# Performance work log

Measured on AMD Instinct MI355X. Metric: run time of the kernel, lower is better.

## Reference

```python
import jax, jax.numpy as jnp
import numpy as np

N_NODES = 100000
N_EDGES = 1250000
IN_NDIM = 128
OUT_NDIM = 64


def setup_inputs() -> dict:
    key = jax.random.key(0)
    ks = jax.random.split(key, 8)
    return {
        "node_feats": jax.random.normal(ks[0], (N_NODES, IN_NDIM), dtype=jnp.float32),
        "edge_d": jax.random.uniform(ks[1], (N_EDGES, 1), dtype=jnp.float32),
        "W0": jax.random.normal(ks[2], (1, 1), dtype=jnp.float32),
        "W1": jax.random.normal(ks[3], (OUT_NDIM, IN_NDIM), dtype=jnp.float32) * (IN_NDIM ** -0.5),
        "W2": jax.random.normal(ks[4], (OUT_NDIM, IN_NDIM), dtype=jnp.float32) * (IN_NDIM ** -0.5),
        "Wa": jax.random.normal(ks[5], (1, 2 * OUT_NDIM + 1), dtype=jnp.float32) * (OUT_NDIM ** -0.5),
        "src": jax.random.randint(ks[6], (N_EDGES,), 0, N_NODES, dtype=jnp.int32),
        "dst": jax.random.randint(ks[7], (N_EDGES,), 0, N_NODES, dtype=jnp.int32),
    }


def reference(node_feats, edge_d, W0, W1, W2, Wa, src, dst):
    N = node_feats.shape[0]
    # fc1 / fc2 node projections (bias-free linears)
    z = node_feats @ W1.T            # [N, out_ndim]
    z_i = node_feats @ W2.T          # [N, out_ndim]
    # fc0 edge feature projection
    t = edge_d @ W0.T                # [E, 1]
    # gather per-edge endpoint features
    z_src = z[src]                   # [E, out_ndim]
    z_dst = z[dst]                   # [E, out_ndim]
    # attention logit: leaky_relu(attn_fc([z_src, z_dst, t]))
    a = jnp.concatenate([z_src, z_dst, t], axis=1) @ Wa.T   # [E, 1]
    e = jax.nn.leaky_relu(a[:, 0], 0.01)                      # torch default slope
    # segment softmax over incoming edges of each dst node
    m = jax.ops.segment_max(e, dst, num_segments=N)          # -inf for empty segs
    ex = jnp.exp(e - m[dst])
    denom = jax.ops.segment_sum(ex, dst, num_segments=N)
    alpha = ex / denom[dst]                                   # [E]
    # weighted scatter-sum of source messages
    z_neighbor = jax.ops.segment_sum(alpha[:, None] * z_src, dst, num_segments=N)
    h = jax.nn.relu(z_i + z_neighbor)
    return h
```

## Files before the change

### kernel.cpp

```cpp
#include <hip/hip_runtime.h>

#define N_NODES 100000
#define N_EDGES 1250000
#define IN_D 128
#define OUT_D 64
#define BSHIFT 8
#define NBUCK  391
#define CAP    4608
#define EPB    4096
#define NBLK_E 306
#define NBLK_G 1563

typedef __attribute__((ext_vector_type(8))) __bf16 bf16x8;
typedef __attribute__((ext_vector_type(4))) float floatx4;

__device__ __forceinline__ float2 up2(unsigned u) {
    return make_float2(__uint_as_float(u << 16),
                       __uint_as_float(u & 0xFFFF0000u));
}

__global__ __launch_bounds__(256) void fusedA_kernel(
    const float* __restrict__ x, const float* __restrict__ W1,
    const float* __restrict__ W2, const float* __restrict__ W0,
    const float* __restrict__ Wa,
    const int* __restrict__ dst, const int* __restrict__ src,
    const float* __restrict__ edge_d,
    int* __restrict__ gcur, uint2* __restrict__ payA,
    unsigned short* __restrict__ zb, unsigned short* __restrict__ zib,
    float* __restrict__ s1, float* __restrict__ s2)
{
    __shared__ __bf16 sB[16384];
    __shared__ float  sWa[128];
    __shared__ int    h[NBUCK];
    __shared__ int    lcur[NBUCK];

    const int t = threadIdx.x;

    if (blockIdx.x < NBLK_E) {
        const float tc = W0[0] * Wa[2 * OUT_D];
        for (int i = t; i < NBUCK; i += 256) h[i] = 0;
        __syncthreads();
        const int base = blockIdx.x * EPB;
        for (int k0 = 0; k0 < EPB; k0 += 1024) {
            int i = base + k0 + t * 4;
            if (i < N_EDGES) {
                int4 d4 = *(const int4*)(dst + i);
                atomicAdd(&h[d4.x >> BSHIFT], 1);
                atomicAdd(&h[d4.y >> BSHIFT], 1);
                atomicAdd(&h[d4.z >> BSHIFT], 1);
                atomicAdd(&h[d4.w >> BSHIFT], 1);
            }
        }
        __syncthreads();
        for (int b = t; b < NBUCK; b += 256) {
            int hc = h[b];
            int p = hc ? atomicAdd(&gcur[b], hc) : 0;
            lcur[b] = b * CAP + p;
        }
        __syncthreads();
        #define EMIT(dv, sv, ev)                                              \
            { int bk = (dv) >> BSHIFT;                                        \
              int pos = atomicAdd(&lcur[bk], 1);                              \
              if (pos < (bk + 1) * CAP)                                       \
                  payA[pos] = make_uint2((unsigned)(sv) |                     \
                                         ((unsigned)((dv) & 255) << 17),      \
                                         __float_as_uint(tc * (ev))); }
        for (int k0 = 0; k0 < EPB; k0 += 1024) {
            int i = base + k0 + t * 4;
            if (i < N_EDGES) {
                int4   d4 = *(const int4*)(dst + i);
                int4   s4 = *(const int4*)(src + i);
                float4 e4 = *(const float4*)(edge_d + i);
                EMIT(d4.x, s4.x, e4.x);
                EMIT(d4.y, s4.y, e4.y);
                EMIT(d4.z, s4.z, e4.z);
                EMIT(d4.w, s4.w, e4.w);
            }
        }
        #undef EMIT
        return;
    }

    #pragma unroll
    for (int g = 0; g < 8; ++g) {
        int gi = t + g * 256;
        int n  = gi >> 4;
        int k8 = gi & 15;
        const float* wrow = (n < 64) ? (W1 + n * 128) : (W2 + (n - 64) * 128);
        float4 v0 = *(const float4*)(wrow + k8 * 8);
        float4 v1 = *(const float4*)(wrow + k8 * 8 + 4);
        int lane = ((k8 & 3) << 4) | (n & 15);
        int off  = (((n >> 4) * 4 + (k8 >> 2)) * 64 + lane) * 8;
        bf16x8 bb;
        bb[0] = (__bf16)v0.x; bb[1] = (__bf16)v0.y;
        bb[2] = (__bf16)v0.z; bb[3] = (__bf16)v0.w;
        bb[4] = (__bf16)v1.x; bb[5] = (__bf16)v1.y;
        bb[6] = (__bf16)v1.z; bb[7] = (__bf16)v1.w;
        *(bf16x8*)(sB + off) = bb;
    }
    if (t < 128) sWa[t] = Wa[t];
    __syncthreads();

    const int lane = t & 63;
    const int wave = t >> 6;
    const int tile = (blockIdx.x - NBLK_E) * 4 + wave;
    if (tile * 16 >= N_NODES) return;

    const int n0 = tile * 16;
    const int m  = lane & 15;
    const int kb = lane >> 4;

    floatx4 acc[8];
    #pragma unroll
    for (int q = 0; q < 8; ++q) acc[q] = (floatx4)(0.f);

    const float* xrow = x + (size_t)(n0 + m) * IN_D;

    #pragma unroll
    for (int kc = 0; kc < 4; ++kc) {
        float4 v0 = *(const float4*)(xrow + kc * 32 + kb * 8);
        float4 v1 = *(const float4*)(xrow + kc * 32 + kb * 8 + 4);
        float xs[8] = {v0.x, v0.y, v0.z, v0.w, v1.x, v1.y, v1.z, v1.w};
        bf16x8 ahi, alo;
        #pragma unroll
        for (int j = 0; j < 8; ++j) {
            __bf16 hh = (__bf16)xs[j];
            ahi[j] = hh;
            alo[j] = (__bf16)(xs[j] - (float)hh);
        }
        #pragma unroll
        for (int nt = 0; nt < 8; ++nt) {
            int off = ((nt * 4 + kc) * 64 + lane) * 8;
            bf16x8 b = *(const bf16x8*)(sB + off);
            acc[nt] = __builtin_amdgcn_mfma_f32_16x16x32_bf16(ahi, b, acc[nt], 0, 0, 0);
            acc[nt] = __builtin_amdgcn_mfma_f32_16x16x32_bf16(alo, b, acc[nt], 0, 0, 0);
        }
    }

    #pragma unroll
    for (int nt = 0; nt < 8; ++nt) {
        int col = (nt & 3) * 16 + m;
        unsigned short* dp = (nt < 4) ? zb : zib;
        #pragma unroll
        for (int reg = 0; reg < 4; ++reg) {
            int row = n0 + kb * 4 + reg;
            __bf16 hh = (__bf16)acc[nt][reg];
            dp[(size_t)row * OUT_D + col] = *(unsigned short*)&hh;
        }
    }

    #pragma unroll
    for (int reg = 0; reg < 4; ++reg) {
        float p1 = 0.f, p2 = 0.f;
        #pragma unroll
        for (int nt = 0; nt < 4; ++nt) {
            float zv = acc[nt][reg];
            p1 += zv * sWa[nt * 16 + m];
            p2 += zv * sWa[64 + nt * 16 + m];
        }
        #pragma unroll
        for (int off = 8; off > 0; off >>= 1) {
            p1 += __shfl_xor(p1, off);
            p2 += __shfl_xor(p2, off);
        }
        if (m == 0) {
            int row = n0 + kb * 4 + reg;
            s1[row] = p1;
            s2[row] = p2;
        }
    }
}

__global__ __launch_bounds__(512) void passB_kernel(
    const int* __restrict__ gcur, const uint2* __restrict__ payA,
    int2* __restrict__ node_meta, uint2* __restrict__ payB)
{
    __shared__ int h[256];
    __shared__ int lc[256];
    __shared__ int sm[256];

    const int b = blockIdx.x, t = threadIdx.x;
    const int base = b * CAP;
    const int cnt = min(gcur[b], CAP);
    const int n0 = b << BSHIFT;

    if (t < 256) h[t] = 0;
    __syncthreads();

    for (int i0 = t * 4; i0 < cnt; i0 += 2048) {
        uint4 u0 = *(const uint4*)(payA + base + i0);
        uint4 u1 = *(const uint4*)(payA + base + i0 + 2);
        atomicAdd(&h[(u0.x >> 17) & 255], 1);
        if (i0 + 1 < cnt) atomicAdd(&h[(u0.z >> 17) & 255], 1);
        if (i0 + 2 < cnt) atomicAdd(&h[(u1.x >> 17) & 255], 1);
        if (i0 + 3 < cnt) atomicAdd(&h[(u1.z >> 17) & 255], 1);
    }
    __syncthreads();

    if (t < 256) {
        int v = h[t];
        sm[t] = v;
        __syncthreads();
        for (int off = 1; off < 256; off <<= 1) {
            int add = (t >= off) ? sm[t - off] : 0;
            __syncthreads();
            sm[t] += add;
            __syncthreads();
        }
        int start = base + sm[t] - v;
        lc[t] = start;
        if (n0 + t < N_NODES) node_meta[n0 + t] = make_int2(start, v);
    } else {
        __syncthreads();
        for (int off = 1; off < 256; off <<= 1) {
            __syncthreads(); __syncthreads();
        }
    }
    __syncthreads();

    #define PUT(xx, yy, ok)                                                   \
        if (ok) { int j = ((xx) >> 17) & 255;                                 \
                  int pos = atomicAdd(&lc[j], 1);                             \
                  payB[pos] = make_uint2((xx) & 0x1FFFFu, (yy)); }
    for (int i0 = t * 4; i0 < cnt; i0 += 2048) {
        uint4 u0 = *(const uint4*)(payA + base + i0);
        uint4 u1 = *(const uint4*)(payA + base + i0 + 2);
        PUT(u0.x, u0.y, true);
        PUT(u0.z, u0.w, i0 + 1 < cnt);
        PUT(u1.x, u1.y, i0 + 2 < cnt);
        PUT(u1.z, u1.w, i0 + 3 < cnt);
    }
    #undef PUT
}

__global__ __launch_bounds__(256) void gather_finalize_kernel(
    const int2* __restrict__ node_meta, const uint2* __restrict__ payB,
    const float* __restrict__ s1, const float* __restrict__ s2,
    const unsigned short* __restrict__ zb, const unsigned short* __restrict__ zib,
    float* __restrict__ out)
{
    __shared__ uint2 buf[8][32];

    const int lane = threadIdx.x & 63;
    const int wave = threadIdx.x >> 6;
    const int half = lane >> 5;
    const int lh   = lane & 31;
    const int nodeSlot = wave * 2 + half;
    const int d = blockIdx.x * 8 + nodeSlot;

    const int2 meta = node_meta[d];
    const int beg = meta.x;
    const int len = meta.y;
    const float s2d = s2[d];

    const int eC = lh >> 3;
    const int c  = lh & 7;

    float den = 0.f;
    float2 a0 = make_float2(0.f, 0.f), a1 = a0, a2 = a0, a3 = a0;

    for (int o = 0; o < len; o += 32) {
        int rem = len - o;
        bool v = lh < rem;
        uint2 p = payB[beg + o + (v ? lh : 0)];
        float ex = 0.f;
        if (v) {
            float a = __uint_as_float(p.y) + s1[p.x] + s2d;
            float e = (a > 0.f) ? a : 0.01f * a;
            ex = __expf(e);
            buf[nodeSlot][lh] = make_uint2(p.x, __float_as_uint(ex));
        }
        den += ex;

        int cnt = min(32, rem);
        for (int g = 0; g * 4 < cnt; ++g) {
            int j = g * 4 + eC;
            uint2 pe = buf[nodeSlot][(j < cnt) ? j : 0];
            float exe = (j < cnt) ? __uint_as_float(pe.y) : 0.f;
            uint4 zv = *(const uint4*)(zb + (size_t)pe.x * OUT_D + c * 8);
            float2 w0 = up2(zv.x), w1 = up2(zv.y), w2 = up2(zv.z), w3 = up2(zv.w);
            a0.x = fmaf(exe, w0.x, a0.x); a0.y = fmaf(exe, w0.y, a0.y);
            a1.x = fmaf(exe, w1.x, a1.x); a1.y = fmaf(exe, w1.y, a1.y);
            a2.x = fmaf(exe, w2.x, a2.x); a2.y = fmaf(exe, w2.y, a2.y);
            a3.x = fmaf(exe, w3.x, a3.x); a3.y = fmaf(exe, w3.y, a3.y);
        }
    }

    #pragma unroll
    for (int off = 16; off > 0; off >>= 1) den += __shfl_xor(den, off);
    #pragma unroll
    for (int off = 8; off <= 16; off <<= 1) {
        a0.x += __shfl_xor(a0.x, off); a0.y += __shfl_xor(a0.y, off);
        a1.x += __shfl_xor(a1.x, off); a1.y += __shfl_xor(a1.y, off);
        a2.x += __shfl_xor(a2.x, off); a2.y += __shfl_xor(a2.y, off);
        a3.x += __shfl_xor(a3.x, off); a3.y += __shfl_xor(a3.y, off);
    }

    if (lh < 8) {
        float inv = (den > 0.f) ? 1.f / den : 0.f;
        uint4 zv = *(const uint4*)(zib + (size_t)d * OUT_D + lh * 8);
        float2 w0 = up2(zv.x), w1 = up2(zv.y), w2 = up2(zv.z), w3 = up2(zv.w);
        float4 o0, o1;
        o0.x = fmaxf(w0.x + a0.x * inv, 0.f);
        o0.y = fmaxf(w0.y + a0.y * inv, 0.f);
        o0.z = fmaxf(w1.x + a1.x * inv, 0.f);
        o0.w = fmaxf(w1.y + a1.y * inv, 0.f);
        o1.x = fmaxf(w2.x + a2.x * inv, 0.f);
        o1.y = fmaxf(w2.y + a2.y * inv, 0.f);
        o1.z = fmaxf(w3.x + a3.x * inv, 0.f);
        o1.w = fmaxf(w3.y + a3.y * inv, 0.f);
        *(float4*)(out + (size_t)d * OUT_D + lh * 8)     = o0;
        *(float4*)(out + (size_t)d * OUT_D + lh * 8 + 4) = o1;
    }
}

extern "C" void kernel_launch(void* const* d_in, const int* in_sizes, int n_in,
                              void* d_out, int out_size, void* d_ws, size_t ws_size,
                              hipStream_t stream) {
    const float* node_feats = (const float*)d_in[0];
    const float* edge_d     = (const float*)d_in[1];
    const float* W0         = (const float*)d_in[2];
    const float* W1         = (const float*)d_in[3];
    const float* W2         = (const float*)d_in[4];
    const float* Wa         = (const float*)d_in[5];
    const int*   src        = (const int*)d_in[6];
    const int*   dst        = (const int*)d_in[7];
    float* out = (float*)d_out;

    char* ws = (char*)d_ws;
    uint2* payA = (uint2*)ws;    ws += (size_t)NBUCK * CAP * 8;
    uint2* payB = (uint2*)ws;    ws += (size_t)NBUCK * CAP * 8;
    unsigned short* zbuf = (unsigned short*)ws; ws += (size_t)N_NODES * OUT_D * 2;
    unsigned short* zib  = (unsigned short*)ws; ws += (size_t)N_NODES * OUT_D * 2;
    float* s1 = (float*)ws;      ws += (size_t)N_NODES * 4;
    float* s2 = (float*)ws;      ws += (size_t)N_NODES * 4;
    int2*  node_meta = (int2*)ws; ws += (size_t)N_NODES * 8;
    int*   gcur = (int*)ws;      ws += ((NBUCK + 3) & ~3) * 4;

    hipMemsetAsync(gcur, 0, NBUCK * 4, stream);

    fusedA_kernel<<<NBLK_E + NBLK_G, 256, 0, stream>>>(
        node_feats, W1, W2, W0, Wa, dst, src, edge_d,
        gcur, payA, zbuf, zib, s1, s2);

    passB_kernel<<<NBUCK, 512, 0, stream>>>(gcur, payA, node_meta, payB);

    gather_finalize_kernel<<<N_NODES / 8, 256, 0, stream>>>(
        node_meta, payB, s1, s2, zbuf, zib, out);
}
```

Before: 191.2 us.

## Fuse bucket sort and gather into one kernel with LDS-resident edge buckets

The second-pass counting sort is merged with the per-node softmax/gather kernel, so each 128-node bucket is sorted into shared memory and consumed in place rather than written to payB and node_meta in global memory. Buckets shrink from 256 to 128 nodes (782 buckets, smaller capacity) so a bucket fits in LDS, and the first pass emits more, smaller blocks. The weight-staging loop is also reindexed so LDS writes are linear. This removes a kernel launch and a global round trip for the sorted edges, but there are only 782 blocks for the gather phase, the large LDS footprint limits occupancy, and overflow of the smaller per-bucket capacity would silently drop edges.

```diff
diff --git a/kernel.cpp b/kernel.cpp
--- a/kernel.cpp
+++ b/kernel.cpp
@@ -4,11 +4,11 @@
 #define N_EDGES 1250000
 #define IN_D 128
 #define OUT_D 64
-#define BSHIFT 8
-#define NBUCK  391
-#define CAP    4608
-#define EPB    4096
-#define NBLK_E 306
+#define BSHIFT 7
+#define NBUCK  782
+#define CAP    2600
+#define EPB    2048
+#define NBLK_E 611
 #define NBLK_G 1563
 
 typedef __attribute__((ext_vector_type(8))) __bf16 bf16x8;
@@ -63,7 +63,7 @@
               int pos = atomicAdd(&lcur[bk], 1);                              \
               if (pos < (bk + 1) * CAP)                                       \
                   payA[pos] = make_uint2((unsigned)(sv) |                     \
-                                         ((unsigned)((dv) & 255) << 17),      \
+                                         ((unsigned)((dv) & 127) << 17),      \
                                          __float_as_uint(tc * (ev))); }
         for (int k0 = 0; k0 < EPB; k0 += 1024) {
             int i = base + k0 + t * 4;
@@ -83,20 +83,22 @@
 
     #pragma unroll
     for (int g = 0; g < 8; ++g) {
-        int gi = t + g * 256;
-        int n  = gi >> 4;
-        int k8 = gi & 15;
+        int idx = t + g * 256;
+        int m  = idx & 15;
+        int kb = (idx >> 4) & 3;
+        int kc = (idx >> 6) & 3;
+        int nt = idx >> 8;
+        int n  = nt * 16 + m;
+        int k8 = kc * 4 + kb;
         const float* wrow = (n < 64) ? (W1 + n * 128) : (W2 + (n - 64) * 128);
         float4 v0 = *(const float4*)(wrow + k8 * 8);
         float4 v1 = *(const float4*)(wrow + k8 * 8 + 4);
-        int lane = ((k8 & 3) << 4) | (n & 15);
-        int off  = (((n >> 4) * 4 + (k8 >> 2)) * 64 + lane) * 8;
         bf16x8 bb;
         bb[0] = (__bf16)v0.x; bb[1] = (__bf16)v0.y;
         bb[2] = (__bf16)v0.z; bb[3] = (__bf16)v0.w;
         bb[4] = (__bf16)v1.x; bb[5] = (__bf16)v1.y;
         bb[6] = (__bf16)v1.z; bb[7] = (__bf16)v1.w;
-        *(bf16x8*)(sB + off) = bb;
+        *(bf16x8*)(sB + idx * 8) = bb;
     }
     if (t < 128) sWa[t] = Wa[t];
     __syncthreads();
@@ -171,146 +173,119 @@
     }
 }
 
-__global__ __launch_bounds__(512) void passB_kernel(
+__global__ __launch_bounds__(256) void bucket_gather_kernel(
     const int* __restrict__ gcur, const uint2* __restrict__ payA,
-    int2* __restrict__ node_meta, uint2* __restrict__ payB)
+    const float* __restrict__ s1, const float* __restrict__ s2,
+    const unsigned short* __restrict__ zb, const unsigned short* __restrict__ zib,
+    float* __restrict__ out)
 {
-    __shared__ int h[256];
-    __shared__ int lc[256];
-    __shared__ int sm[256];
+    __shared__ uint2 buf[CAP];
+    __shared__ int h[128], st[128], lc[128], sm[128];
 
     const int b = blockIdx.x, t = threadIdx.x;
     const int base = b * CAP;
     const int cnt = min(gcur[b], CAP);
     const int n0 = b << BSHIFT;
 
-    if (t < 256) h[t] = 0;
-    __syncthreads();
-
-    for (int i0 = t * 4; i0 < cnt; i0 += 2048) {
-        uint4 u0 = *(const uint4*)(payA + base + i0);
-        uint4 u1 = *(const uint4*)(payA + base + i0 + 2);
-        atomicAdd(&h[(u0.x >> 17) & 255], 1);
-        if (i0 + 1 < cnt) atomicAdd(&h[(u0.z >> 17) & 255], 1);
-        if (i0 + 2 < cnt) atomicAdd(&h[(u1.x >> 17) & 255], 1);
-        if (i0 + 3 < cnt) atomicAdd(&h[(u1.z >> 17) & 255], 1);
-    }
-    __syncthreads();
-
-    if (t < 256) {
-        int v = h[t];
-        sm[t] = v;
-        __syncthreads();
-        for (int off = 1; off < 256; off <<= 1) {
-            int add = (t >= off) ? sm[t - off] : 0;
-            __syncthreads();
-            sm[t] += add;
-            __syncthreads();
-        }
-        int start = base + sm[t] - v;
-        lc[t] = start;
-        if (n0 + t < N_NODES) node_meta[n0 + t] = make_int2(start, v);
-    } else {
-        __syncthreads();
-        for (int off = 1; off < 256; off <<= 1) {
-            __syncthreads(); __syncthreads();
-        }
-    }
-    __syncthreads();
-
-    #define PUT(xx, yy, ok)                                                   \
-        if (ok) { int j = ((xx) >> 17) & 255;                                 \
-                  int pos = atomicAdd(&lc[j], 1);                             \
-                  payB[pos] = make_uint2((xx) & 0x1FFFFu, (yy)); }
-    for (int i0 = t * 4; i0 < cnt; i0 += 2048) {
-        uint4 u0 = *(const uint4*)(payA + base + i0);
-        uint4 u1 = *(const uint4*)(payA + base + i0 + 2);
-        PUT(u0.x, u0.y, true);
-        PUT(u0.z, u0.w, i0 + 1 < cnt);
-        PUT(u1.x, u1.y, i0 + 2 < cnt);
-        PUT(u1.z, u1.w, i0 + 3 < cnt);
-    }
-    #undef PUT
-}
-
-__global__ __launch_bounds__(256) void gather_finalize_kernel(
-    const int2* __restrict__ node_meta, const uint2* __restrict__ payB,
-    const float* __restrict__ s1, const float* __restrict__ s2,
-    const unsigned short* __restrict__ zb, const unsigned short* __restrict__ zib,
-    float* __restrict__ out)
-{
-    __shared__ uint2 buf[8][32];
-
-    const int lane = threadIdx.x & 63;
-    const int wave = threadIdx.x >> 6;
-    const int half = lane >> 5;
-    const int lh   = lane & 31;
-    const int nodeSlot = wave * 2 + half;
-    const int d = blockIdx.x * 8 + nodeSlot;
-
-    const int2 meta = node_meta[d];
-    const int beg = meta.x;
-    const int len = meta.y;
-    const float s2d = s2[d];
-
-    const int eC = lh >> 3;
-    const int c  = lh & 7;
-
-    float den = 0.f;
-    float2 a0 = make_float2(0.f, 0.f), a1 = a0, a2 = a0, a3 = a0;
-
-    for (int o = 0; o < len; o += 32) {
-        int rem = len - o;
-        bool v = lh < rem;
-        uint2 p = payB[beg + o + (v ? lh : 0)];
-        float ex = 0.f;
-        if (v) {
-            float a = __uint_as_float(p.y) + s1[p.x] + s2d;
-            float e = (a > 0.f) ? a : 0.01f * a;
-            ex = __expf(e);
-            buf[nodeSlot][lh] = make_uint2(p.x, __float_as_uint(ex));
-        }
-        den += ex;
-
-        int cnt = min(32, rem);
-        for (int g = 0; g * 4 < cnt; ++g) {
-            int j = g * 4 + eC;
-            uint2 pe = buf[nodeSlot][(j < cnt) ? j : 0];
-            float exe = (j < cnt) ? __uint_as_float(pe.y) : 0.f;
-            uint4 zv = *(const uint4*)(zb + (size_t)pe.x * OUT_D + c * 8);
+    if (t < 128) h[t] = 0;
+    __syncthreads();
+    for (int i0 = t * 2; i0 < cnt; i0 += 512) {
+        uint4 u = *(const uint4*)(payA + base + i0);
+        atomicAdd(&h[(u.x >> 17) & 127], 1);
+        if (i0 + 1 < cnt) atomicAdd(&h[(u.z >> 17) & 127], 1);
+    }
+    __syncthreads();
+
+    if (t < 128) sm[t] = h[t];
+    __syncthreads();
+    for (int off = 1; off < 128; off <<= 1) {
+        int add = 0;
+        if (t < 128 && t >= off) add = sm[t - off];
+        __syncthreads();
+        if (t < 128) sm[t] += add;
+        __syncthreads();
+    }
+    if (t < 128) { int s_ = sm[t] - h[t]; st[t] = s_; lc[t] = s_; }
+    __syncthreads();
+
+    for (int i0 = t * 2; i0 < cnt; i0 += 512) {
+        uint4 u = *(const uint4*)(payA + base + i0);
+        int j0 = (u.x >> 17) & 127;
+        int p0 = atomicAdd(&lc[j0], 1);
+        buf[p0] = make_uint2(u.x & 0x1FFFFu, u.y);
+        if (i0 + 1 < cnt) {
+            int j1 = (u.z >> 17) & 127;
+            int p1 = atomicAdd(&lc[j1], 1);
+            buf[p1] = make_uint2(u.z & 0x1FFFFu, u.w);
+        }
+    }
+    __syncthreads();
+
+    const int slot = t >> 5;
+    const int lh   = t & 31;
+    const int eC   = lh >> 3;
+    const int c    = lh & 7;
+
+    for (int j = slot; j < 128; j += 8) {
+        int d = n0 + j;
+        if (d >= N_NODES) break;
+        const int beg = st[j];
+        const int len = h[j];
+        const float s2d = s2[d];
+
+        float den = 0.f;
+        float2 a0 = make_float2(0.f, 0.f), a1 = a0, a2 = a0, a3 = a0;
+
+        for (int o = 0; o < len; o += 32) {
+            int rem = len - o;
+            if (lh < rem) {
+                uint2 p = buf[beg + o + lh];
+                float a = __uint_as_float(p.y) + s1[p.x] + s2d;
+                float e = (a > 0.f) ? a : 0.01f * a;
+                float ex = __expf(e);
+                den += ex;
+                buf[beg + o + lh].y = __float_as_uint(ex);
+            }
+            int cc = min(32, rem);
+            for (int g = 0; g * 4 < cc; ++g) {
+                int j2 = g * 4 + eC;
+                uint2 pe = buf[beg + o + ((j2 < cc) ? j2 : 0)];
+                float exe = (j2 < cc) ? __uint_as_float(pe.y) : 0.f;
+                uint4 zv = *(const uint4*)(zb + (size_t)pe.x * OUT_D + c * 8);
+                float2 w0 = up2(zv.x), w1 = up2(zv.y), w2 = up2(zv.z), w3 = up2(zv.w);
+                a0.x = fmaf(exe, w0.x, a0.x); a0.y = fmaf(exe, w0.y, a0.y);
+                a1.x = fmaf(exe, w1.x, a1.x); a1.y = fmaf(exe, w1.y, a1.y);
+                a2.x = fmaf(exe, w2.x, a2.x); a2.y = fmaf(exe, w2.y, a2.y);
+                a3.x = fmaf(exe, w3.x, a3.x); a3.y = fmaf(exe, w3.y, a3.y);
+            }
+        }
+
+        #pragma unroll
+        for (int off = 16; off > 0; off >>= 1) den += __shfl_xor(den, off);
+        #pragma unroll
+        for (int off = 8; off <= 16; off <<= 1) {
+            a0.x += __shfl_xor(a0.x, off); a0.y += __shfl_xor(a0.y, off);
+            a1.x += __shfl_xor(a1.x, off); a1.y += __shfl_xor(a1.y, off);
+            a2.x += __shfl_xor(a2.x, off); a2.y += __shfl_xor(a2.y, off);
+            a3.x += __shfl_xor(a3.x, off); a3.y += __shfl_xor(a3.y, off);
+        }
+
+        if (lh < 8) {
+            float inv = (den > 0.f) ? 1.f / den : 0.f;
+            uint4 zv = *(const uint4*)(zib + (size_t)d * OUT_D + lh * 8);
             float2 w0 = up2(zv.x), w1 = up2(zv.y), w2 = up2(zv.z), w3 = up2(zv.w);
-            a0.x = fmaf(exe, w0.x, a0.x); a0.y = fmaf(exe, w0.y, a0.y);
-            a1.x = fmaf(exe, w1.x, a1.x); a1.y = fmaf(exe, w1.y, a1.y);
-            a2.x = fmaf(exe, w2.x, a2.x); a2.y = fmaf(exe, w2.y, a2.y);
-            a3.x = fmaf(exe, w3.x, a3.x); a3.y = fmaf(exe, w3.y, a3.y);
-        }
-    }
-
-    #pragma unroll
-    for (int off = 16; off > 0; off >>= 1) den += __shfl_xor(den, off);
-    #pragma unroll
-    for (int off = 8; off <= 16; off <<= 1) {
-        a0.x += __shfl_xor(a0.x, off); a0.y += __shfl_xor(a0.y, off);
-        a1.x += __shfl_xor(a1.x, off); a1.y += __shfl_xor(a1.y, off);
-        a2.x += __shfl_xor(a2.x, off); a2.y += __shfl_xor(a2.y, off);
-        a3.x += __shfl_xor(a3.x, off); a3.y += __shfl_xor(a3.y, off);
-    }
-
-    if (lh < 8) {
-        float inv = (den > 0.f) ? 1.f / den : 0.f;
-        uint4 zv = *(const uint4*)(zib + (size_t)d * OUT_D + lh * 8);
-        float2 w0 = up2(zv.x), w1 = up2(zv.y), w2 = up2(zv.z), w3 = up2(zv.w);
-        float4 o0, o1;
-        o0.x = fmaxf(w0.x + a0.x * inv, 0.f);
-        o0.y = fmaxf(w0.y + a0.y * inv, 0.f);
-        o0.z = fmaxf(w1.x + a1.x * inv, 0.f);
-        o0.w = fmaxf(w1.y + a1.y * inv, 0.f);
-        o1.x = fmaxf(w2.x + a2.x * inv, 0.f);
-        o1.y = fmaxf(w2.y + a2.y * inv, 0.f);
-        o1.z = fmaxf(w3.x + a3.x * inv, 0.f);
-        o1.w = fmaxf(w3.y + a3.y * inv, 0.f);
-        *(float4*)(out + (size_t)d * OUT_D + lh * 8)     = o0;
-        *(float4*)(out + (size_t)d * OUT_D + lh * 8 + 4) = o1;
+            float4 o0, o1;
+            o0.x = fmaxf(w0.x + a0.x * inv, 0.f);
+            o0.y = fmaxf(w0.y + a0.y * inv, 0.f);
+            o0.z = fmaxf(w1.x + a1.x * inv, 0.f);
+            o0.w = fmaxf(w1.y + a1.y * inv, 0.f);
+            o1.x = fmaxf(w2.x + a2.x * inv, 0.f);
+            o1.y = fmaxf(w2.y + a2.y * inv, 0.f);
+            o1.z = fmaxf(w3.x + a3.x * inv, 0.f);
+            o1.w = fmaxf(w3.y + a3.y * inv, 0.f);
+            *(float4*)(out + (size_t)d * OUT_D + lh * 8)     = o0;
+            *(float4*)(out + (size_t)d * OUT_D + lh * 8 + 4) = o1;
+        }
     }
 }
 
@@ -329,12 +304,10 @@
 
     char* ws = (char*)d_ws;
     uint2* payA = (uint2*)ws;    ws += (size_t)NBUCK * CAP * 8;
-    uint2* payB = (uint2*)ws;    ws += (size_t)NBUCK * CAP * 8;
     unsigned short* zbuf = (unsigned short*)ws; ws += (size_t)N_NODES * OUT_D * 2;
     unsigned short* zib  = (unsigned short*)ws; ws += (size_t)N_NODES * OUT_D * 2;
     float* s1 = (float*)ws;      ws += (size_t)N_NODES * 4;
     float* s2 = (float*)ws;      ws += (size_t)N_NODES * 4;
-    int2*  node_meta = (int2*)ws; ws += (size_t)N_NODES * 8;
     int*   gcur = (int*)ws;      ws += ((NBUCK + 3) & ~3) * 4;
 
     hipMemsetAsync(gcur, 0, NBUCK * 4, stream);
@@ -343,8 +316,6 @@
         node_feats, W1, W2, W0, Wa, dst, src, edge_d,
         gcur, payA, zbuf, zib, s1, s2);
 
-    passB_kernel<<<NBUCK, 512, 0, stream>>>(gcur, payA, node_meta, payB);
-
-    gather_finalize_kernel<<<N_NODES / 8, 256, 0, stream>>>(
-        node_meta, payB, s1, s2, zbuf, zib, out);
+    bucket_gather_kernel<<<NBUCK, 256, 0, stream>>>(
+        gcur, payA, s1, s2, zbuf, zib, out);
 }
```

Measured after the change: 214.7 us. 1.12x slower.
